# Kernel tuning notes

Hardware: AMD Instinct MI355X
Metric: run time of the kernel (lower is better)

## Reference

```python
import jax, jax.numpy as jnp
import numpy as np

N, D, P, NS = 2048, 64, 32, 512  # nnodes, stop_embedding_size, preference_dim, n_active_stops
LEAKY_SLOPE = 0.01
COS_EPS = 1e-8


def setup_inputs() -> dict:
    key = jax.random.key(0)
    ks = jax.random.split(key, 10)
    dist = jax.random.uniform(ks[0], (N, N), dtype=jnp.float32)
    stops = jax.random.randint(ks[1], (NS,), 0, N)
    emb_w = jax.random.normal(ks[2], (N, D), dtype=jnp.float32) * 0.05      # nn.Embedding weight
    lin_l_w = jax.random.normal(ks[3], (P, D), dtype=jnp.float32) * 0.05    # SAGEConv lin_l (aggregated)
    lin_l_b = jnp.zeros((P,), dtype=jnp.float32)
    lin_r_w = jax.random.normal(ks[4], (P, D), dtype=jnp.float32) * 0.05    # SAGEConv lin_r (root)
    edge_w = jax.random.normal(ks[5], (2 * P,), dtype=jnp.float32) * 0.05   # edge_summarizer weight
    edge_b = jnp.zeros((), dtype=jnp.float32)
    in_len = 2 * N + 3 + P
    comb_w = jax.random.normal(ks[6], (N, in_len), dtype=jnp.float32) * 0.02  # combiner weight
    comb_b = jnp.zeros((N,), dtype=jnp.float32)
    return {
        "dist": dist, "emb_w": emb_w,
        "lin_l_w": lin_l_w, "lin_l_b": lin_l_b, "lin_r_w": lin_r_w,
        "edge_w": edge_w, "edge_b": edge_b,
        "comb_w": comb_w, "comb_b": comb_b,
        "stops": stops, "weekday": 3, "vehicles": 5,
    }


def reference(dist, emb_w, lin_l_w, lin_l_b, lin_r_w, edge_w, edge_b,
              comb_w, comb_b, stops, weekday, vehicles):
    dt = emb_w.dtype
    # --- cosine-similarity graph build ---
    norm = jnp.maximum(jnp.linalg.norm(emb_w, axis=1, keepdims=True), COS_EPS)
    xn = emb_w / norm
    sim = xn @ xn.T                                   # [N, N]
    sim = sim * (1.0 - jnp.eye(N, dtype=dt))          # fill_diagonal_(0)
    keep = jnp.zeros((N,), dtype=bool).at[stops].set(True)
    adj = ((sim > 0.5) & keep[:, None] & keep[None, :]).astype(dt)  # [N, N]
    # --- SAGEConv (mean aggregation): lin_l(mean_j x_j) + lin_r(x_i) ---
    deg = jnp.maximum(adj.sum(axis=1, keepdims=True), 1.0)
    agg = (adj @ emb_w) / deg                         # [N, D]
    pref = agg @ lin_l_w.T + lin_l_b + emb_w @ lin_r_w.T   # [N, P]
    # --- all-pairs edge summaries: Linear([pref_i, pref_j]) + LeakyReLU ---
    # equivalent to concat-then-linear, without materializing [N^2, 2P]
    a = pref @ edge_w[:P]                             # [N]
    b = pref @ edge_w[P:]                             # [N]
    es = a[:, None] + b[None, :] + edge_b             # [N, N]
    es = jnp.where(es >= 0, es, LEAKY_SLOPE * es)
    # --- combiner + log-softmax ---
    weekday_feat = jnp.full((N, 1), weekday, dtype=dt)
    vehicle_feat = jnp.full((N, 1), vehicles, dtype=dt)
    stop_feat = keep.astype(dt)[:, None]
    combined = jnp.concatenate([pref, es, dist, weekday_feat, vehicle_feat, stop_feat], axis=1)
    out = combined @ comb_w.T + comb_b                # [N, N]
    return jax.nn.log_softmax(out, axis=1)
```

## Files before the change

kernel.cpp:

```cpp
#include <hip/hip_runtime.h>

typedef unsigned short u16;
typedef __attribute__((ext_vector_type(8))) short bf16x8;
typedef __attribute__((ext_vector_type(4))) float f32x4;

__device__ __forceinline__ u16 f2bf(float f) {
    return (u16)((__float_as_uint(f) + 0x8000u) >> 16);
}

#define N_NODES 2048
#define D_EMB 64
#define P_DIM 32
#define NS_STOPS 512
#define IN_LEN 4131
#define NKT 65

#define SWZ(row, c) ((((row) * 8) + ((c) ^ ((row) & 7))) * 8)

__device__ __forceinline__ void gload16(const u16* g, u16* l) {
    __builtin_amdgcn_global_load_lds((const __attribute__((address_space(1))) void*)g,
                                     (__attribute__((address_space(3))) void*)l, 16, 0, 0);
}

__global__ __launch_bounds__(256) void k_prep(const float* __restrict__ emb, const int* __restrict__ stops,
                                              float* __restrict__ xn, int* __restrict__ keep,
                                              int* __restrict__ klist, int* __restrict__ knum) {
    int t = threadIdx.x;
    if (blockIdx.x < 512) {
        int row = blockIdx.x * 4 + (t >> 6);
        int d = t & 63;
        float v = emb[row * D_EMB + d];
        float s = v * v;
        #pragma unroll
        for (int off = 32; off; off >>= 1) s += __shfl_xor(s, off, 64);
        float nm = fmaxf(sqrtf(s), 1e-8f);
        xn[row * D_EMB + d] = v / nm;
    } else {
        __shared__ int cnt;
        if (t == 0) cnt = 0;
        for (int n = t; n < N_NODES; n += 256) keep[n] = 0;
        __syncthreads();
        for (int u = t; u < NS_STOPS; u += 256) keep[stops[u]] = 1;
        __syncthreads();
        for (int n = t; n < N_NODES; n += 256)
            if (keep[n]) { int p = atomicAdd(&cnt, 1); klist[p] = n; }
        __syncthreads();
        if (t == 0) *knum = cnt;
    }
}

__global__ __launch_bounds__(256) void k_aggpref(const float* __restrict__ xn, const float* __restrict__ emb,
                                                 const int* __restrict__ keep, const int* __restrict__ klist,
                                                 const int* __restrict__ knum,
                                                 const float* __restrict__ lin_l_w, const float* __restrict__ lin_l_b,
                                                 const float* __restrict__ lin_r_w, const float* __restrict__ edge_w,
                                                 float* __restrict__ pref, float* __restrict__ av, float* __restrict__ bv) {
    int i = blockIdx.x, t = threadIdx.x;
    __shared__ float xi[D_EMB];
    __shared__ float embL[D_EMB];
    __shared__ float aggL[D_EMB];
    __shared__ int degL;
    int ki = keep[i];
    if (t < D_EMB) { xi[t] = xn[i * D_EMB + t]; embL[t] = emb[i * D_EMB + t]; aggL[t] = 0.f; }
    if (t == 0) degL = 0;
    __syncthreads();
    if (ki) {
        int nk = knum[0];
        const f32x4* xiv = (const f32x4*)xi;
        for (int u = t; u < nk; u += 256) {
            int j = klist[u];
            if (j == i) continue;
            const f32x4* xj = (const f32x4*)&xn[j * D_EMB];
            f32x4 dv = {0.f, 0.f, 0.f, 0.f};
            #pragma unroll
            for (int d = 0; d < 16; ++d) dv += xiv[d] * xj[d];
            float dot = dv[0] + dv[1] + dv[2] + dv[3];
            if (dot > 0.5f) {
                atomicAdd(&degL, 1);
                #pragma unroll
                for (int d = 0; d < D_EMB; ++d) atomicAdd(&aggL[d], emb[j * D_EMB + d]);
            }
        }
    }
    __syncthreads();
    if (t < D_EMB) {
        float deg = fmaxf((float)degL, 1.0f);
        aggL[t] = ki ? (aggL[t] / deg) : 0.f;
    }
    __syncthreads();
    if (t < P_DIM) {
        float s = lin_l_b[t];
        const float* wl = &lin_l_w[t * D_EMB];
        const float* wr = &lin_r_w[t * D_EMB];
        #pragma unroll
        for (int d = 0; d < D_EMB; ++d) s += aggL[d] * wl[d] + embL[d] * wr[d];
        pref[i * P_DIM + t] = s;
        float a = s * edge_w[t];
        float b = s * edge_w[P_DIM + t];
        #pragma unroll
        for (int off = 16; off; off >>= 1) { a += __shfl_xor(a, off, 64); b += __shfl_xor(b, off, 64); }
        if (t == 0) { av[i] = a; bv[i] = b; }
    }
}

__global__ __launch_bounds__(256) void k_pack(const float* __restrict__ comb_w, const float* __restrict__ comb_b,
                                              const int* __restrict__ wk_p, const int* __restrict__ vh_p,
                                              const float* __restrict__ dist, const float* __restrict__ pref,
                                              const float* __restrict__ av, const float* __restrict__ bv,
                                              const float* __restrict__ edge_b,
                                              u16* __restrict__ Bp, u16* __restrict__ Ap,
                                              float* __restrict__ cvec, float* __restrict__ w3) {
    int bid = blockIdx.x, t = threadIdx.x;
    if (bid < 2048) {
        int j = bid;
        int nt = j >> 7, r = j & 127;
        const float* cw = comb_w + (size_t)j * IN_LEN;
        for (int q = t; q < 520; q += 256) {
            int kt = q >> 3, c = q & 7;
            int k0 = q * 8;
            bf16x8 v;
            if (k0 < 4096) {
                f32x4 f0, f1;
                __builtin_memcpy(&f0, cw + 32 + k0, 16);
                __builtin_memcpy(&f1, cw + 36 + k0, 16);
                #pragma unroll
                for (int e = 0; e < 4; ++e) { v[e] = (short)f2bf(f0[e]); v[4 + e] = (short)f2bf(f1[e]); }
            } else if (k0 < 4128) {
                f32x4 f0, f1;
                __builtin_memcpy(&f0, cw + (k0 - 4096), 16);
                __builtin_memcpy(&f1, cw + (k0 - 4092), 16);
                #pragma unroll
                for (int e = 0; e < 4; ++e) { v[e] = (short)f2bf(f0[e]); v[4 + e] = (short)f2bf(f1[e]); }
            } else {
                #pragma unroll
                for (int e = 0; e < 8; ++e) v[e] = 0;
            }
            size_t off = (((size_t)nt * NKT + kt) * 128 + r) * 64 + (size_t)((c ^ (r & 7)) * 8);
            *(bf16x8*)&Bp[off] = v;
        }
        if (t == 0) {
            float wk = (float)wk_p[0], vh = (float)vh_p[0];
            cvec[j] = wk * cw[4128] + vh * cw[4129] + comb_b[j];
            w3[j] = cw[4130];
        }
    } else {
        int row = bid - 2048;
        int rt = row >> 6, r = row & 63;
        float ab = av[row] + edge_b[0];
        const float* drow = dist + (size_t)row * 2048;
        const float* prow = pref + (size_t)row * P_DIM;
        for (int q = t; q < 520; q += 256) {
            int kt = q >> 3, c = q & 7;
            int k0 = q * 8;
            bf16x8 v;
            if (k0 < 2048) {
                const f32x4* bp = (const f32x4*)(bv + k0);
                f32x4 f0 = bp[0], f1 = bp[1];
                #pragma unroll
                for (int e = 0; e < 4; ++e) {
                    float s0 = ab + f0[e]; s0 = (s0 >= 0.f) ? s0 : 0.01f * s0;
                    float s1 = ab + f1[e]; s1 = (s1 >= 0.f) ? s1 : 0.01f * s1;
                    v[e] = (short)f2bf(s0); v[4 + e] = (short)f2bf(s1);
                }
            } else if (k0 < 4096) {
                const f32x4* dp = (const f32x4*)(drow + (k0 - 2048));
                f32x4 f0 = dp[0], f1 = dp[1];
                #pragma unroll
                for (int e = 0; e < 4; ++e) { v[e] = (short)f2bf(f0[e]); v[4 + e] = (short)f2bf(f1[e]); }
            } else if (k0 < 4128) {
                const f32x4* pp = (const f32x4*)(prow + (k0 - 4096));
                f32x4 f0 = pp[0], f1 = pp[1];
                #pragma unroll
                for (int e = 0; e < 4; ++e) { v[e] = (short)f2bf(f0[e]); v[4 + e] = (short)f2bf(f1[e]); }
            } else {
                #pragma unroll
                for (int e = 0; e < 8; ++e) v[e] = 0;
            }
            size_t off = (((size_t)rt * NKT + kt) * 64 + r) * 64 + (size_t)((c ^ (r & 7)) * 8);
            *(bf16x8*)&Ap[off] = v;
        }
    }
}

__global__ __launch_bounds__(256) void k_gemm_d(const u16* __restrict__ Ap, const u16* __restrict__ Bp,
                                                float* __restrict__ Cout) {
    __shared__ __attribute__((aligned(16))) short As[2][64 * 64];
    __shared__ __attribute__((aligned(16))) short Bs[2][128 * 64];
    int t = threadIdx.x;
    int mt = blockIdx.y, nt = blockIdx.x;
    int tileM = mt * 64, tileN = nt * 128;
    int lane = t & 63;
    int wid = t >> 6;
    int waveM = wid & 1, waveN = wid >> 1;
    int l16 = lane & 15, quad = lane >> 4;

    f32x4 acc[2][4];
    #pragma unroll
    for (int a_ = 0; a_ < 2; ++a_)
        #pragma unroll
        for (int b_ = 0; b_ < 4; ++b_) acc[a_][b_] = (f32x4){0.f, 0.f, 0.f, 0.f};

    const u16* ga = Ap + ((size_t)mt * NKT) * 4096 + t * 8;
    const u16* gb = Bp + ((size_t)nt * NKT) * 8192 + t * 8;

    {
        u16* ad = (u16*)As[0] + t * 8;
        u16* bd = (u16*)Bs[0] + t * 8;
        gload16(ga, ad);
        gload16(ga + 2048, ad + 2048);
        #pragma unroll
        for (int u = 0; u < 4; ++u) gload16(gb + u * 2048, bd + u * 2048);
    }

    int cur = 0;
    for (int kt = 0; kt < NKT; ++kt) {
        __syncthreads();
        if (kt + 1 < NKT) {
            const u16* gan = ga + (size_t)(kt + 1) * 4096;
            const u16* gbn = gb + (size_t)(kt + 1) * 8192;
            u16* ad = (u16*)As[cur ^ 1] + t * 8;
            u16* bd = (u16*)Bs[cur ^ 1] + t * 8;
            gload16(gan, ad);
            gload16(gan + 2048, ad + 2048);
            #pragma unroll
            for (int u = 0; u < 4; ++u) gload16(gbn + u * 2048, bd + u * 2048);
        }
        const short* Asc = As[cur];
        const short* Bsc = Bs[cur];
        #pragma unroll
        for (int kk = 0; kk < 64; kk += 32) {
            int cbase = kk >> 3;
            bf16x8 af[2], bfr[4];
            #pragma unroll
            for (int mi = 0; mi < 2; ++mi) {
                int row = waveM * 32 + mi * 16 + l16;
                af[mi] = *(const bf16x8*)&Asc[SWZ(row, cbase + quad)];
            }
            #pragma unroll
            for (int ni = 0; ni < 4; ++ni) {
                int row = waveN * 64 + ni * 16 + l16;
                bfr[ni] = *(const bf16x8*)&Bsc[SWZ(row, cbase + quad)];
            }
            #pragma unroll
            for (int mi = 0; mi < 2; ++mi)
                #pragma unroll
                for (int ni = 0; ni < 4; ++ni)
                    acc[mi][ni] = __builtin_amdgcn_mfma_f32_16x16x32_bf16(af[mi], bfr[ni], acc[mi][ni], 0, 0, 0);
        }
        cur ^= 1;
    }
    #pragma unroll
    for (int mi = 0; mi < 2; ++mi)
        #pragma unroll
        for (int ni = 0; ni < 4; ++ni) {
            int row = tileM + waveM * 32 + mi * 16 + quad * 4;
            int col = tileN + waveN * 64 + ni * 16 + l16;
            float* cp = Cout + (size_t)row * N_NODES + col;
            #pragma unroll
            for (int rr = 0; rr < 4; ++rr) cp[(size_t)rr * N_NODES] = acc[mi][ni][rr];
        }
}

__global__ __launch_bounds__(256) void k_epi(const float* __restrict__ cvec, const float* __restrict__ w3,
                                             const int* __restrict__ keep, float* __restrict__ out) {
    int i = blockIdx.x, t = threadIdx.x;
    __shared__ float redmax[4], redsum[4];
    float ki = keep[i] ? 1.f : 0.f;
    f32x4* orow = (f32x4*)(out + (size_t)i * N_NODES);
    const f32x4* cv = (const f32x4*)cvec;
    const f32x4* wv = (const f32x4*)w3;
    f32x4 v0 = orow[t] + cv[t] + ki * wv[t];
    f32x4 v1 = orow[t + 256] + cv[t + 256] + ki * wv[t + 256];
    float vmax = fmaxf(fmaxf(fmaxf(v0[0], v0[1]), fmaxf(v0[2], v0[3])),
                       fmaxf(fmaxf(v1[0], v1[1]), fmaxf(v1[2], v1[3])));
    #pragma unroll
    for (int off = 32; off; off >>= 1) vmax = fmaxf(vmax, __shfl_xor(vmax, off, 64));
    if ((t & 63) == 0) redmax[t >> 6] = vmax;
    __syncthreads();
    vmax = fmaxf(fmaxf(redmax[0], redmax[1]), fmaxf(redmax[2], redmax[3]));
    float se = 0.f;
    #pragma unroll
    for (int e = 0; e < 4; ++e) se += expf(v0[e] - vmax) + expf(v1[e] - vmax);
    #pragma unroll
    for (int off = 32; off; off >>= 1) se += __shfl_xor(se, off, 64);
    if ((t & 63) == 0) redsum[t >> 6] = se;
    __syncthreads();
    se = redsum[0] + redsum[1] + redsum[2] + redsum[3];
    float lz = vmax + logf(se);
    orow[t] = v0 - lz;
    orow[t + 256] = v1 - lz;
}

extern "C" void kernel_launch(void* const* d_in, const int* in_sizes, int n_in,
                              void* d_out, int out_size, void* d_ws, size_t ws_size,
                              hipStream_t stream) {
    const float* dist    = (const float*)d_in[0];
    const float* emb     = (const float*)d_in[1];
    const float* lin_l_w = (const float*)d_in[2];
    const float* lin_l_b = (const float*)d_in[3];
    const float* lin_r_w = (const float*)d_in[4];
    const float* edge_w  = (const float*)d_in[5];
    const float* edge_b  = (const float*)d_in[6];
    const float* comb_w  = (const float*)d_in[7];
    const float* comb_b  = (const float*)d_in[8];
    const int* stops     = (const int*)d_in[9];
    const int* wk        = (const int*)d_in[10];
    const int* vh        = (const int*)d_in[11];

    char* ws = (char*)d_ws;
    float* xn    = (float*)(ws + 0);
    int*   keep  = (int*)(ws + 524288);
    float* pref  = (float*)(ws + 532480);
    float* av    = (float*)(ws + 794624);
    float* bv    = (float*)(ws + 802816);
    float* cvec  = (float*)(ws + 811008);
    float* w3    = (float*)(ws + 819200);
    int*   klist = (int*)(ws + 827392);
    int*   knum  = (int*)(ws + 835584);
    u16*   Ap    = (u16*)(ws + 843776);
    u16*   Bp    = (u16*)(ws + 17883136);
    float* out   = (float*)d_out;

    hipLaunchKernelGGL(k_prep,    dim3(513),      dim3(256), 0, stream, emb, stops, xn, keep, klist, knum);
    hipLaunchKernelGGL(k_aggpref, dim3(2048),     dim3(256), 0, stream, xn, emb, keep, klist, knum,
                       lin_l_w, lin_l_b, lin_r_w, edge_w, pref, av, bv);
    hipLaunchKernelGGL(k_pack,    dim3(4096),     dim3(256), 0, stream, comb_w, comb_b, wk, vh,
                       dist, pref, av, bv, edge_b, Bp, Ap, cvec, w3);
    hipLaunchKernelGGL(k_gemm_d,  dim3(16, 32),   dim3(256), 0, stream, Ap, Bp, out);
    hipLaunchKernelGGL(k_epi,     dim3(2048),     dim3(256), 0, stream, cvec, w3, keep, out);
}
```

Measured before the change: 196.6 us.

## Fuse prep kernel into aggregation by rebuilding stop bitmask per block

```diff
diff --git a/kernel.cpp b/kernel.cpp
--- a/kernel.cpp
+++ b/kernel.cpp
@@ -22,63 +22,70 @@
                                      (__attribute__((address_space(3))) void*)l, 16, 0, 0);
 }
 
-__global__ __launch_bounds__(256) void k_prep(const float* __restrict__ emb, const int* __restrict__ stops,
-                                              float* __restrict__ xn, int* __restrict__ keep,
-                                              int* __restrict__ klist, int* __restrict__ knum) {
-    int t = threadIdx.x;
-    if (blockIdx.x < 512) {
-        int row = blockIdx.x * 4 + (t >> 6);
-        int d = t & 63;
-        float v = emb[row * D_EMB + d];
-        float s = v * v;
-        #pragma unroll
-        for (int off = 32; off; off >>= 1) s += __shfl_xor(s, off, 64);
-        float nm = fmaxf(sqrtf(s), 1e-8f);
-        xn[row * D_EMB + d] = v / nm;
-    } else {
-        __shared__ int cnt;
-        if (t == 0) cnt = 0;
-        for (int n = t; n < N_NODES; n += 256) keep[n] = 0;
-        __syncthreads();
-        for (int u = t; u < NS_STOPS; u += 256) keep[stops[u]] = 1;
-        __syncthreads();
-        for (int n = t; n < N_NODES; n += 256)
-            if (keep[n]) { int p = atomicAdd(&cnt, 1); klist[p] = n; }
-        __syncthreads();
-        if (t == 0) *knum = cnt;
-    }
-}
-
-__global__ __launch_bounds__(256) void k_aggpref(const float* __restrict__ xn, const float* __restrict__ emb,
-                                                 const int* __restrict__ keep, const int* __restrict__ klist,
-                                                 const int* __restrict__ knum,
+__global__ __launch_bounds__(256) void k_aggpref(const float* __restrict__ emb, const int* __restrict__ stops,
                                                  const float* __restrict__ lin_l_w, const float* __restrict__ lin_l_b,
                                                  const float* __restrict__ lin_r_w, const float* __restrict__ edge_w,
                                                  float* __restrict__ pref, float* __restrict__ av, float* __restrict__ bv) {
     int i = blockIdx.x, t = threadIdx.x;
+    __shared__ int bm[64];
+    __shared__ int kl[NS_STOPS];
+    __shared__ int cnt, degL;
     __shared__ float xi[D_EMB];
-    __shared__ float embL[D_EMB];
     __shared__ float aggL[D_EMB];
-    __shared__ int degL;
-    int ki = keep[i];
-    if (t < D_EMB) { xi[t] = xn[i * D_EMB + t]; embL[t] = emb[i * D_EMB + t]; aggL[t] = 0.f; }
-    if (t == 0) degL = 0;
-    __syncthreads();
+    __shared__ float niS;
+    if (t < 64) bm[t] = 0;
+    if (t == 0) { cnt = 0; degL = 0; }
+    if (t < D_EMB) { xi[t] = emb[i * D_EMB + t]; aggL[t] = 0.f; }
+    __syncthreads();
+    {
+        int s0 = stops[t], s1 = stops[t + 256];
+        atomicOr(&bm[s0 >> 5], 1 << (s0 & 31));
+        atomicOr(&bm[s1 >> 5], 1 << (s1 & 31));
+    }
+    __syncthreads();
+    {
+        int w = bm[t >> 2];
+        int base = (t >> 2) * 32 + (t & 3) * 8;
+        #pragma unroll
+        for (int e = 0; e < 8; ++e)
+            if ((w >> ((t & 3) * 8 + e)) & 1) { int p = atomicAdd(&cnt, 1); kl[p] = base + e; }
+    }
+    if (t < 64) {
+        float s = xi[t] * xi[t];
+        #pragma unroll
+        for (int off = 32; off; off >>= 1) s += __shfl_xor(s, off, 64);
+        if (t == 0) niS = fmaxf(sqrtf(s), 1e-8f);
+    }
+    __syncthreads();
+    int ki = (bm[i >> 5] >> (i & 31)) & 1;
     if (ki) {
-        int nk = knum[0];
+        int nk = cnt;
+        float ni = niS;
         const f32x4* xiv = (const f32x4*)xi;
         for (int u = t; u < nk; u += 256) {
-            int j = klist[u];
+            int j = kl[u];
             if (j == i) continue;
-            const f32x4* xj = (const f32x4*)&xn[j * D_EMB];
+            const f32x4* ej = (const f32x4*)&emb[j * D_EMB];
+            f32x4 er[16];
             f32x4 dv = {0.f, 0.f, 0.f, 0.f};
-            #pragma unroll
-            for (int d = 0; d < 16; ++d) dv += xiv[d] * xj[d];
+            f32x4 sv = {0.f, 0.f, 0.f, 0.f};
+            #pragma unroll
+            for (int d = 0; d < 16; ++d) {
+                er[d] = ej[d];
+                dv += xiv[d] * er[d];
+                sv += er[d] * er[d];
+            }
             float dot = dv[0] + dv[1] + dv[2] + dv[3];
-            if (dot > 0.5f) {
+            float nj = fmaxf(sqrtf(sv[0] + sv[1] + sv[2] + sv[3]), 1e-8f);
+            if (dot > 0.5f * ni * nj) {
                 atomicAdd(&degL, 1);
                 #pragma unroll
-                for (int d = 0; d < D_EMB; ++d) atomicAdd(&aggL[d], emb[j * D_EMB + d]);
+                for (int d = 0; d < 16; ++d) {
+                    atomicAdd(&aggL[d * 4 + 0], er[d][0]);
+                    atomicAdd(&aggL[d * 4 + 1], er[d][1]);
+                    atomicAdd(&aggL[d * 4 + 2], er[d][2]);
+                    atomicAdd(&aggL[d * 4 + 3], er[d][3]);
+                }
             }
         }
     }
@@ -93,7 +100,7 @@
         const float* wl = &lin_l_w[t * D_EMB];
         const float* wr = &lin_r_w[t * D_EMB];
         #pragma unroll
-        for (int d = 0; d < D_EMB; ++d) s += aggL[d] * wl[d] + embL[d] * wr[d];
+        for (int d = 0; d < D_EMB; ++d) s += aggL[d] * wl[d] + xi[d] * wr[d];
         pref[i * P_DIM + t] = s;
         float a = s * edge_w[t];
         float b = s * edge_w[P_DIM + t];
@@ -262,10 +269,19 @@
 }
 
 __global__ __launch_bounds__(256) void k_epi(const float* __restrict__ cvec, const float* __restrict__ w3,
-                                             const int* __restrict__ keep, float* __restrict__ out) {
+                                             const int* __restrict__ stops, float* __restrict__ out) {
     int i = blockIdx.x, t = threadIdx.x;
+    __shared__ int bm[64];
     __shared__ float redmax[4], redsum[4];
-    float ki = keep[i] ? 1.f : 0.f;
+    if (t < 64) bm[t] = 0;
+    __syncthreads();
+    {
+        int s0 = stops[t], s1 = stops[t + 256];
+        atomicOr(&bm[s0 >> 5], 1 << (s0 & 31));
+        atomicOr(&bm[s1 >> 5], 1 << (s1 & 31));
+    }
+    __syncthreads();
+    float ki = (float)((bm[i >> 5] >> (i & 31)) & 1);
     f32x4* orow = (f32x4*)(out + (size_t)i * N_NODES);
     const f32x4* cv = (const f32x4*)cvec;
     const f32x4* wv = (const f32x4*)w3;
@@ -308,24 +324,19 @@
     const int* vh        = (const int*)d_in[11];
 
     char* ws = (char*)d_ws;
-    float* xn    = (float*)(ws + 0);
-    int*   keep  = (int*)(ws + 524288);
-    float* pref  = (float*)(ws + 532480);
-    float* av    = (float*)(ws + 794624);
-    float* bv    = (float*)(ws + 802816);
-    float* cvec  = (float*)(ws + 811008);
-    float* w3    = (float*)(ws + 819200);
-    int*   klist = (int*)(ws + 827392);
-    int*   knum  = (int*)(ws + 835584);
-    u16*   Ap    = (u16*)(ws + 843776);
-    u16*   Bp    = (u16*)(ws + 17883136);
+    float* pref  = (float*)(ws + 0);
+    float* av    = (float*)(ws + 262144);
+    float* bv    = (float*)(ws + 270336);
+    float* cvec  = (float*)(ws + 278528);
+    float* w3    = (float*)(ws + 286720);
+    u16*   Ap    = (u16*)(ws + 294912);
+    u16*   Bp    = (u16*)(ws + 17334272);
     float* out   = (float*)d_out;
 
-    hipLaunchKernelGGL(k_prep,    dim3(513),      dim3(256), 0, stream, emb, stops, xn, keep, klist, knum);
-    hipLaunchKernelGGL(k_aggpref, dim3(2048),     dim3(256), 0, stream, xn, emb, keep, klist, knum,
+    hipLaunchKernelGGL(k_aggpref, dim3(2048),   dim3(256), 0, stream, emb, stops,
                        lin_l_w, lin_l_b, lin_r_w, edge_w, pref, av, bv);
-    hipLaunchKernelGGL(k_pack,    dim3(4096),     dim3(256), 0, stream, comb_w, comb_b, wk, vh,
+    hipLaunchKernelGGL(k_pack,    dim3(4096),   dim3(256), 0, stream, comb_w, comb_b, wk, vh,
                        dist, pref, av, bv, edge_b, Bp, Ap, cvec, w3);
-    hipLaunchKernelGGL(k_gemm_d,  dim3(16, 32),   dim3(256), 0, stream, Ap, Bp, out);
-    hipLaunchKernelGGL(k_epi,     dim3(2048),     dim3(256), 0, stream, cvec, w3, keep, out);
-}
+    hipLaunchKernelGGL(k_gemm_d,  dim3(16, 32), dim3(256), 0, stream, Ap, Bp, out);
+    hipLaunchKernelGGL(k_epi,     dim3(2048),   dim3(256), 0, stream, cvec, w3, stops, out);
+}
```

Result: no change. 196.3 us (-0.1%).
